# Kernel optimization log

Measured on AMD Instinct MI355X. Metric: run time of the kernel, lower is better.

The kernel has to match this reference:

```python
import jax, jax.numpy as jnp
import numpy as np

# Key insight: 'take the first candidate in descending-score order that is not yet
# used' is exactly 'argmax of the score over unused items'. Since vocab == 25 and
# every index has a char, the Python fallback branch is unreachable for
# seq_len <= vocab. So the whole greedy dedup collapses to a masked-argmax scan
# over positions, vectorized across the batch.

def setup_inputs() -> dict:
    key = jax.random.key(0)
    B, S, V = 65536, 25, 25
    matrix = jax.random.normal(key, (B, S, V), dtype=jnp.float32)
    return {"matrix": matrix}


def reference(matrix):
    B, S, V = matrix.shape
    neg = jnp.finfo(matrix.dtype).min

    def step(used, scores):  # used: [B,V] bool, scores: [B,V]
        masked = jnp.where(used, neg, scores)
        sel = jnp.argmax(masked, axis=-1)                       # [B] greedy pick
        val = jnp.take_along_axis(scores, sel[:, None], axis=-1)[:, 0]
        used = used | jax.nn.one_hot(sel, V, dtype=bool)        # mark as used
        return used, (sel, val)

    used0 = jnp.zeros((B, V), dtype=bool)
    _, (sels, vals) = jax.lax.scan(step, used0, jnp.swapaxes(matrix, 0, 1))
    # actions: [B,S] int32 item ids (== char index, char = chr(id + ord('A')))
    actions = jnp.swapaxes(sels, 0, 1).astype(jnp.int32)
    sel_scores = jnp.swapaxes(vals, 0, 1)                        # [B,S] float
    return actions, sel_scores
```

## Files before the change

kernel.cpp:

```cpp
#include <hip/hip_runtime.h>


#define SLEN 25
#define VOCAB 25

__global__ __launch_bounds__(256) void greedy_dedup_kernel(
    const float* __restrict__ m, float* __restrict__ out, int B) {
  int b = blockIdx.x * blockDim.x + threadIdx.x;
  if (b >= B) return;

  const float* row = m + (long long)b * (SLEN * VOCAB);
  float* act_out = out + (long long)b * SLEN;
  float* val_out = out + (long long)B * SLEN + (long long)b * SLEN;

  float cur[VOCAB];
  float nxt[VOCAB];

#pragma unroll
  for (int v = 0; v < VOCAB; ++v) cur[v] = row[v];

  unsigned used = 0u;

  for (int s = 0; s < SLEN; ++s) {
    if (s + 1 < SLEN) {
      const float* p = row + (s + 1) * VOCAB;
#pragma unroll
      for (int v = 0; v < VOCAB; ++v) nxt[v] = p[v];
    }

    float best = -3.402823466e38f;
    int bi = 0;
#pragma unroll
    for (int v = 0; v < VOCAB; ++v) {
      bool free_v = ((used >> v) & 1u) == 0u;
      if (free_v && cur[v] > best) { best = cur[v]; bi = v; }
    }

    used |= (1u << bi);
    act_out[s] = (float)bi;
    val_out[s] = best;

#pragma unroll
    for (int v = 0; v < VOCAB; ++v) cur[v] = nxt[v];
  }
}

extern "C" void kernel_launch(void* const* d_in, const int* in_sizes, int n_in,
                              void* d_out, int out_size, void* d_ws, size_t ws_size,
                              hipStream_t stream) {
  const float* m = (const float*)d_in[0];
  float* out = (float*)d_out;
  int B = in_sizes[0] / (SLEN * VOCAB);

  int block = 256;
  int grid = (B + block - 1) / block;
  greedy_dedup_kernel<<<grid, block, 0, stream>>>(m, out, B);
}
```

Before: 271.8 us.

## Stage row tiles in LDS via coalesced global_load_lds with double buffering

Each block now loads one sequence step for its 256 rows cooperatively. Consecutive lanes fetch consecutive dwords straight into LDS with global_load_lds, double-buffered so the next step's load overlaps the current step's argmax. Previously each thread read its own row at a large stride. Results are staged in LDS and written out coalesced. The trade-off is about 100KB of LDS per block, which limits occupancy, plus a block barrier every step. The grid also assumes B is a multiple of 256.

```diff
diff --git a/kernel.cpp b/kernel.cpp
--- a/kernel.cpp
+++ b/kernel.cpp
@@ -1,47 +1,83 @@
 #include <hip/hip_runtime.h>
+#include <stdint.h>
 
 
-#define SLEN 25
+#define S_LEN 25
 #define VOCAB 25
+#define ROWS_PER_BLOCK 256
+#define THREADS 256
+#define WAVES 4
+#define DW_PER_STEP (ROWS_PER_BLOCK * VOCAB)
+#define DW_PER_WAVE (DW_PER_STEP / WAVES)
+#define J_ITERS (DW_PER_WAVE / 64)
 
-__global__ __launch_bounds__(256) void greedy_dedup_kernel(
+__device__ __forceinline__ void gld_dword(const float* g, float* l) {
+  __builtin_amdgcn_global_load_lds(
+      (const __attribute__((address_space(1))) void*)g,
+      (__attribute__((address_space(3))) void*)l, 4, 0, 0);
+}
+
+__global__ __launch_bounds__(THREADS) void greedy_dedup_kernel(
     const float* __restrict__ m, float* __restrict__ out, int B) {
-  int b = blockIdx.x * blockDim.x + threadIdx.x;
-  if (b >= B) return;
+  __shared__ float buf[2][DW_PER_STEP];
+  __shared__ float actbuf[DW_PER_STEP];
+  __shared__ float valbuf[DW_PER_STEP];
 
-  const float* row = m + (long long)b * (SLEN * VOCAB);
-  float* act_out = out + (long long)b * SLEN;
-  float* val_out = out + (long long)B * SLEN + (long long)b * SLEN;
+  const int t = threadIdx.x;
+  const int lane = t & 63;
+  const int wv = t >> 6;
+  const long long blk0 = (long long)blockIdx.x * ROWS_PER_BLOCK;
+  const float* bb = m + blk0 * (S_LEN * VOCAB);
 
-  float cur[VOCAB];
-  float nxt[VOCAB];
+  const float* ga[J_ITERS];
+#pragma unroll
+  for (int j = 0; j < J_ITERS; ++j) {
+    int linear = wv * DW_PER_WAVE + j * 64 + lane;
+    int row = linear / VOCAB;
+    int v = linear - row * VOCAB;
+    ga[j] = bb + row * (S_LEN * VOCAB) + v;
+  }
 
 #pragma unroll
-  for (int v = 0; v < VOCAB; ++v) cur[v] = row[v];
+  for (int j = 0; j < J_ITERS; ++j) {
+    gld_dword(ga[j], &buf[0][wv * DW_PER_WAVE + j * 64]);
+    ga[j] += VOCAB;
+  }
+  __syncthreads();
 
   unsigned used = 0u;
-
-  for (int s = 0; s < SLEN; ++s) {
-    if (s + 1 < SLEN) {
-      const float* p = row + (s + 1) * VOCAB;
+  for (int s = 0; s < S_LEN; ++s) {
+    if (s + 1 < S_LEN) {
+      float* dst = buf[(s + 1) & 1];
 #pragma unroll
-      for (int v = 0; v < VOCAB; ++v) nxt[v] = p[v];
+      for (int j = 0; j < J_ITERS; ++j) {
+        gld_dword(ga[j], &dst[wv * DW_PER_WAVE + j * 64]);
+        ga[j] += VOCAB;
+      }
     }
 
+    const float* src = buf[s & 1] + t * VOCAB;
     float best = -3.402823466e38f;
     int bi = 0;
 #pragma unroll
     for (int v = 0; v < VOCAB; ++v) {
+      float x = src[v];
       bool free_v = ((used >> v) & 1u) == 0u;
-      if (free_v && cur[v] > best) { best = cur[v]; bi = v; }
+      if (free_v && x > best) { best = x; bi = v; }
     }
+    used |= (1u << bi);
+    actbuf[t * VOCAB + s] = (float)bi;
+    valbuf[t * VOCAB + s] = best;
+    __syncthreads();
+  }
 
-    used |= (1u << bi);
-    act_out[s] = (float)bi;
-    val_out[s] = best;
-
+  float* gact = out + blk0 * S_LEN;
+  float* gval = out + (long long)B * S_LEN + blk0 * S_LEN;
 #pragma unroll
-    for (int v = 0; v < VOCAB; ++v) cur[v] = nxt[v];
+  for (int k = 0; k < S_LEN; ++k) {
+    int idx = t + k * THREADS;
+    gact[idx] = actbuf[idx];
+    gval[idx] = valbuf[idx];
   }
 }
 
@@ -50,9 +86,7 @@
                               hipStream_t stream) {
   const float* m = (const float*)d_in[0];
   float* out = (float*)d_out;
-  int B = in_sizes[0] / (SLEN * VOCAB);
-
-  int block = 256;
-  int grid = (B + block - 1) / block;
-  greedy_dedup_kernel<<<grid, block, 0, stream>>>(m, out, B);
+  int B = in_sizes[0] / (S_LEN * VOCAB);
+  int grid = B / ROWS_PER_BLOCK;
+  greedy_dedup_kernel<<<grid, THREADS, 0, stream>>>(m, out, B);
 }
```

Result: faster. 244.5 us (-10.0%).

## Stage rows through LDS with coalesced float4 loads and split argmax across lanes

Applied to the files above, without the earlier changes.

Each block of 128 threads now copies 32 batch rows into shared memory with coalesced float4 loads. Two lanes then share each row's 25-way argmax, each scanning about half the vocab, and combine their results with a cross-lane shuffle. Outputs are staged in LDS and written back coalesced. This replaces the strided per-thread global reads and writes of the old kernel. In exchange it uses 80KB of LDS per block and leaves only 64 of 128 threads busy during compute. It also assumes B is divisible by 32, and the lane halves overlap at index 12.

```diff
diff --git a/kernel.cpp b/kernel.cpp
--- a/kernel.cpp
+++ b/kernel.cpp
@@ -1,47 +1,93 @@
 #include <hip/hip_runtime.h>
+#include <float.h>
 
 
-#define SLEN 25
+#define S_LEN 25
 #define VOCAB 25
+#define ROWS 32
+#define THREADS 128
+#define ROW_DW (S_LEN * VOCAB)
+#define BLK_DW (ROWS * ROW_DW)
+#define NV4 40
+#define OUT_DW (ROWS * S_LEN)
 
-__global__ __launch_bounds__(256) void greedy_dedup_kernel(
+__global__ __launch_bounds__(THREADS) void greedy_dedup_kernel(
     const float* __restrict__ m, float* __restrict__ out, int B) {
-  int b = blockIdx.x * blockDim.x + threadIdx.x;
-  if (b >= B) return;
+  __shared__ float buf[BLK_DW];
 
-  const float* row = m + (long long)b * (SLEN * VOCAB);
-  float* act_out = out + (long long)b * SLEN;
-  float* val_out = out + (long long)B * SLEN + (long long)b * SLEN;
+  const int t = threadIdx.x;
+  const long long blk = blockIdx.x;
+  const float* src = m + blk * (long long)BLK_DW;
 
-  float cur[VOCAB];
-  float nxt[VOCAB];
+  float4 v[NV4];
+#pragma unroll
+  for (int i = 0; i < NV4; ++i) {
+    int dw = (i * THREADS + t) * 4;
+    if (dw < BLK_DW) v[i] = *(const float4*)(src + dw);
+  }
+#pragma unroll
+  for (int i = 0; i < NV4; ++i) {
+    int dw = (i * THREADS + t) * 4;
+    if (dw < BLK_DW) *(float4*)(&buf[dw]) = v[i];
+  }
+  __syncthreads();
+
+  if (t < 64) {
+    const int r = t & 31;
+    const int hi = t >> 5;
+    const int vbase = hi * 12;
+    const float* myrow = &buf[r * ROW_DW];
+
+    unsigned used = 0u;
+    float acts[S_LEN], vals[S_LEN];
+
+    float cur[13], nxt[13];
+#pragma unroll
+    for (int j = 0; j < 13; ++j) cur[j] = myrow[vbase + j];
 
 #pragma unroll
-  for (int v = 0; v < VOCAB; ++v) cur[v] = row[v];
+    for (int s = 0; s < S_LEN; ++s) {
+      if (s + 1 < S_LEN) {
+#pragma unroll
+        for (int j = 0; j < 13; ++j) nxt[j] = myrow[(s + 1) * VOCAB + vbase + j];
+      }
 
-  unsigned used = 0u;
+      float best = -FLT_MAX;
+      int bi = VOCAB;
+#pragma unroll
+      for (int j = 0; j < 13; ++j) {
+        int vv = vbase + j;
+        bool free_v = ((used >> vv) & 1u) == 0u;
+        if (free_v && cur[j] > best) { best = cur[j]; bi = vv; }
+      }
 
-  for (int s = 0; s < SLEN; ++s) {
-    if (s + 1 < SLEN) {
-      const float* p = row + (s + 1) * VOCAB;
+      float obest = __shfl_xor(best, 32);
+      int obi = __shfl_xor(bi, 32);
+      if (obest > best || (obest == best && obi < bi)) { best = obest; bi = obi; }
+
+      used |= (1u << bi);
+      acts[s] = (float)bi;
+      vals[s] = best;
+
 #pragma unroll
-      for (int v = 0; v < VOCAB; ++v) nxt[v] = p[v];
+      for (int j = 0; j < 13; ++j) cur[j] = nxt[j];
     }
 
-    float best = -3.402823466e38f;
-    int bi = 0;
+    if (t < 32) {
 #pragma unroll
-    for (int v = 0; v < VOCAB; ++v) {
-      bool free_v = ((used >> v) & 1u) == 0u;
-      if (free_v && cur[v] > best) { best = cur[v]; bi = v; }
+      for (int s = 0; s < S_LEN; ++s) {
+        buf[r * S_LEN + s] = acts[s];
+        buf[OUT_DW + r * S_LEN + s] = vals[s];
+      }
     }
+  }
+  __syncthreads();
 
-    used |= (1u << bi);
-    act_out[s] = (float)bi;
-    val_out[s] = best;
-
-#pragma unroll
-    for (int v = 0; v < VOCAB; ++v) cur[v] = nxt[v];
+  float* gact = out + blk * OUT_DW;
+  float* gval = out + (long long)B * S_LEN + blk * OUT_DW;
+  for (int idx = t; idx < OUT_DW; idx += THREADS) {
+    gact[idx] = buf[idx];
+    gval[idx] = buf[OUT_DW + idx];
   }
 }
 
@@ -50,9 +96,7 @@
                               hipStream_t stream) {
   const float* m = (const float*)d_in[0];
   float* out = (float*)d_out;
-  int B = in_sizes[0] / (SLEN * VOCAB);
-
-  int block = 256;
-  int grid = (B + block - 1) / block;
-  greedy_dedup_kernel<<<grid, block, 0, stream>>>(m, out, B);
+  int B = in_sizes[0] / ROW_DW;
+  int grid = B / ROWS;
+  greedy_dedup_kernel<<<grid, THREADS, 0, stream>>>(m, out, B);
 }
```

New measurement: 334.4 us. 1.23x slower.
